# Performance work log

Measured on AMD Instinct MI355X. Metric: run time of the kernel, lower is better.

The kernel has to match this reference:

```python
import jax, jax.numpy as jnp
import numpy as np

K = 32  # attention rank
EPS = 1e-6

def setup_inputs() -> dict:
    key = jax.random.key(0)
    k1, k2 = jax.random.split(key)
    N, d = 500000, 256
    x = jax.random.normal(k1, (N, d), dtype=jnp.float32)
    # Xavier-normal-ish scale for Linear(d, 4k)
    W = jax.random.normal(k2, (d, 4 * K), dtype=jnp.float32) * jnp.sqrt(2.0 / (d + 4 * K))
    b = jnp.zeros((4 * K,), dtype=jnp.float32)
    return {"x": x, "W": W, "b": b}

def reference(x, W, b):
    # X = ReLU(x @ W + b): [N, 4k]
    X = jax.nn.relu(x @ W + b)
    U = X[:, :K]            # [N, k]
    V = X[:, K:2 * K]       # [N, k]
    Z = X[:, 2 * K:3 * K]   # [N, k]
    T = X[:, 3 * K:]        # [N, k]
    # joint_normalize2: norm_factor = sum(U @ (V^T @ ones)) / N + eps
    s = V.sum(axis=0)                              # [k] == V^T @ ones
    norm_factor = (U @ s).sum() / U.shape[0] + EPS  # scalar
    D = 1.0 / norm_factor
    # low-rank attention: U @ (V^T @ Z), inner [k, k] GEMM kept tiny
    VtZ = jnp.einsum('nk,nj->kj', V, Z)  # [k, k]
    res = U @ VtZ                        # [N, k]
    return jnp.concatenate((res * D, T), axis=1)  # [N, 2k]
```

## Files before the change

kernel.cpp:

```cpp
#include <hip/hip_runtime.h>
#include <hip/hip_bf16.h>

#define DK 256
#define NC 128
#define EPSV 1e-6f

typedef __bf16 bf16x8 __attribute__((ext_vector_type(8)));
typedef __bf16 bf16x4 __attribute__((ext_vector_type(4)));
typedef float f32x4 __attribute__((ext_vector_type(4)));


__global__ __launch_bounds__(512, 4) void k_gemm(
    const float* __restrict__ x, const float* __restrict__ W,
    const float* __restrict__ bias, float* __restrict__ out,
    float* __restrict__ accg, int N)
{
  __shared__ __bf16 Wlds[32768];
  __shared__ __bf16 Vt[32 * 72];
  __shared__ __bf16 Zt[32 * 72];
  __shared__ float  redS[64];

  const int tid  = threadIdx.x;
  const int wave = tid >> 6;
  const int lane = tid & 63;
  const int quad = lane >> 4;
  const int l16  = lane & 15;
  const int mw   = wave >> 1;
  const int nw   = wave & 1;

  for (int f = tid; f < 4096; f += 512) {
    const int n  = f & 127;
    const int qk = f >> 7;
    const int k0 = (qk >> 2) * 32 + (qk & 3) * 8;
    bf16x8 w;
    #pragma unroll
    for (int j = 0; j < 8; ++j) w[j] = (__bf16)W[(size_t)(k0 + j) * NC + n];
    *(bf16x8*)&Wlds[f * 8] = w;
  }
  float bias4[4];
  #pragma unroll
  for (int ntl = 0; ntl < 4; ++ntl) bias4[ntl] = bias[nw * 64 + ntl * 16 + l16];
  __syncthreads();

  float usumv[2] = {0.f, 0.f};
  float ssumv[2] = {0.f, 0.f};
  f32x4 vacc = (f32x4){0.f, 0.f, 0.f, 0.f};
  const int mt = wave >> 1, nt = wave & 1;

  const int nchunks = (N + 63) >> 6;
  for (int c = blockIdx.x; c < nchunks; c += gridDim.x) {
    const int rbase = c << 6;
    const int arow  = rbase + mw * 16 + l16;
    const bool rv   = arow < N;
    const float* xr = x + (size_t)arow * DK;

    f32x4 xv[16];
    #pragma unroll
    for (int kk = 0; kk < 8; ++kk) {
      const int koff = kk * 32 + quad * 8;
      xv[2 * kk]     = rv ? *(const f32x4*)(xr + koff)     : (f32x4){0.f,0.f,0.f,0.f};
      xv[2 * kk + 1] = rv ? *(const f32x4*)(xr + koff + 4) : (f32x4){0.f,0.f,0.f,0.f};
    }

    f32x4 acc[4];
    #pragma unroll
    for (int t = 0; t < 4; ++t) acc[t] = (f32x4){0.f, 0.f, 0.f, 0.f};

    #pragma unroll
    for (int kk = 0; kk < 8; ++kk) {
      bf16x8 af;
      af[0] = (__bf16)xv[2*kk].x;   af[1] = (__bf16)xv[2*kk].y;
      af[2] = (__bf16)xv[2*kk].z;   af[3] = (__bf16)xv[2*kk].w;
      af[4] = (__bf16)xv[2*kk+1].x; af[5] = (__bf16)xv[2*kk+1].y;
      af[6] = (__bf16)xv[2*kk+1].z; af[7] = (__bf16)xv[2*kk+1].w;
      #pragma unroll
      for (int ntl = 0; ntl < 4; ++ntl) {
        const bf16x8 bf = *(const bf16x8*)&Wlds[(((kk << 2) | quad) * 128
                                                + nw * 64 + ntl * 16 + l16) * 8];
        acc[ntl] = __builtin_amdgcn_mfma_f32_16x16x32_bf16(af, bf, acc[ntl], 0, 0, 0);
      }
    }

    #pragma unroll
    for (int ntl = 0; ntl < 4; ++ntl) {
      float v4[4];
      #pragma unroll
      for (int r = 0; r < 4; ++r) {
        const int grow = rbase + mw * 16 + quad * 4 + r;
        float v = acc[ntl][r] + bias4[ntl];
        v = fmaxf(v, 0.f);
        if (grow >= N) v = 0.f;
        v4[r] = v;
      }
      const int grow0 = rbase + mw * 16 + quad * 4;
      if (nw == 0) {
        if (ntl < 2) {
          #pragma unroll
          for (int r = 0; r < 4; ++r) {
            if (grow0 + r < N) out[(size_t)(grow0 + r) * 64 + ntl * 16 + l16] = v4[r];
            usumv[ntl] += v4[r];
          }
        } else {
          ssumv[ntl - 2] += v4[0] + v4[1] + v4[2] + v4[3];
          bf16x4 pv;
          pv[0] = (__bf16)v4[0]; pv[1] = (__bf16)v4[1];
          pv[2] = (__bf16)v4[2]; pv[3] = (__bf16)v4[3];
          const int col = (ntl - 2) * 16 + l16;
          const int lrow = mw * 16 + quad * 4;
          *(bf16x4*)&Vt[col * 72 + lrow] = pv;
        }
      } else {
        if (ntl < 2) {
          bf16x4 pv;
          pv[0] = (__bf16)v4[0]; pv[1] = (__bf16)v4[1];
          pv[2] = (__bf16)v4[2]; pv[3] = (__bf16)v4[3];
          const int col = ntl * 16 + l16;
          const int lrow = mw * 16 + quad * 4;
          *(bf16x4*)&Zt[col * 72 + lrow] = pv;
        } else {
          #pragma unroll
          for (int r = 0; r < 4; ++r)
            if (grow0 + r < N) out[(size_t)(grow0 + r) * 64 + 32 + (ntl - 2) * 16 + l16] = v4[r];
        }
      }
    }
    __syncthreads();
    if (wave < 4) {
      #pragma unroll
      for (int ks = 0; ks < 2; ++ks) {
        const bf16x8 av = *(const bf16x8*)&Vt[(mt * 16 + l16) * 72 + ks * 32 + quad * 8];
        const bf16x8 bz = *(const bf16x8*)&Zt[(nt * 16 + l16) * 72 + ks * 32 + quad * 8];
        vacc = __builtin_amdgcn_mfma_f32_16x16x32_bf16(av, bz, vacc, 0, 0, 0);
      }
    }
    __syncthreads();
  }

  if (tid < 64) redS[tid] = 0.f;
  __syncthreads();
  if (nw == 0) {
    atomicAdd(&redS[l16],      usumv[0]);
    atomicAdd(&redS[16 + l16], usumv[1]);
    atomicAdd(&redS[32 + l16], ssumv[0]);
    atomicAdd(&redS[48 + l16], ssumv[1]);
  }
  __syncthreads();
  if (tid < 64) atomicAdd(&accg[tid], redS[tid]);
  if (wave < 4) {
    #pragma unroll
    for (int r = 0; r < 4; ++r)
      atomicAdd(&accg[64 + (mt * 16 + quad * 4 + r) * 32 + nt * 16 + l16], vacc[r]);
  }
}

__global__ void k_norm(float* __restrict__ accg, int N) {
  const int t = threadIdx.x;
  float p = 0.f;
  if (t < 32) p = accg[t] * accg[32 + t];
  #pragma unroll
  for (int off = 16; off >= 1; off >>= 1) p += __shfl_down(p, off);
  if (t == 0) accg[1088] = 1.0f / (p / (float)N + EPSV);
}

__global__ __launch_bounds__(256) void k_res(float* __restrict__ out,
                                             const float* __restrict__ accg, int N) {
  __shared__ float Ms[32 * 33];
  __shared__ float Us[64 * 33];
  const float D = accg[1088];
  for (int i = threadIdx.x; i < 1024; i += 256)
    Ms[(i >> 5) * 33 + (i & 31)] = accg[64 + i] * D;
  const int j  = threadIdx.x & 31;
  const int r0 = threadIdx.x >> 5;
  const int rbase = blockIdx.x * 64;
  #pragma unroll
  for (int i = 0; i < 8; ++i) {
    const int lr = r0 + i * 8;
    const int row = rbase + lr;
    Us[lr * 33 + j] = (row < N) ? out[(size_t)row * 64 + j] : 0.f;
  }
  __syncthreads();
  #pragma unroll
  for (int i = 0; i < 8; ++i) {
    const int lr = r0 + i * 8;
    const int row = rbase + lr;
    if (row < N) {
      float a = 0.f;
      #pragma unroll
      for (int k = 0; k < 32; ++k) a += Us[lr * 33 + k] * Ms[k * 33 + j];
      out[(size_t)row * 64 + j] = a;
    }
  }
}

extern "C" void kernel_launch(void* const* d_in, const int* in_sizes, int n_in,
                              void* d_out, int out_size, void* d_ws, size_t ws_size,
                              hipStream_t stream) {
  const float* x    = (const float*)d_in[0];
  const float* W    = (const float*)d_in[1];
  const float* b    = (const float*)d_in[2];
  float* out  = (float*)d_out;
  float* accg = (float*)d_ws;
  const int N = in_sizes[0] / DK;
  const int ngroups = (N + 63) >> 6;

  hipMemsetAsync(accg, 0, 1089 * sizeof(float), stream);
  hipLaunchKernelGGL(k_gemm, dim3(512),     dim3(512), 0, stream, x, W, b, out, accg, N);
  hipLaunchKernelGGL(k_norm, dim3(1),       dim3(64),  0, stream, accg, N);
  hipLaunchKernelGGL(k_res,  dim3(ngroups), dim3(256), 0, stream, out, accg, N);
}
```

Measured before the change: 784.7 us.

## Give each wave full-width row tiles with private V/Z buffers, dropping per-chunk barriers

Each wave now computes all 128 output columns for its own 16 rows, using 1024-thread blocks and 256-row chunks. The V^T·Z product is accumulated from per-wave LDS scratch, so the two block-wide barriers per chunk are gone. X loads are split into two halves so the second half can overlap with the first half's MFMAs. Per-block V^T·Z partials go to workspace and a new reduction kernel sums them and computes the norm factor. In exchange it uses much more LDS and registers per block, allows only one block per CU with a 256-block grid, and adds a partial-sum write plus a reduction pass.

```diff
diff --git a/kernel.cpp b/kernel.cpp
--- a/kernel.cpp
+++ b/kernel.cpp
@@ -2,164 +2,189 @@
 #include <hip/hip_bf16.h>
 
 #define DK 256
-#define NC 128
 #define EPSV 1e-6f
+#define CHUNK 256
+#define GGRID 256
 
 typedef __bf16 bf16x8 __attribute__((ext_vector_type(8)));
 typedef __bf16 bf16x4 __attribute__((ext_vector_type(4)));
 typedef float f32x4 __attribute__((ext_vector_type(4)));
 
 
-__global__ __launch_bounds__(512, 4) void k_gemm(
+
+__global__ __launch_bounds__(1024) void k_gemm(
     const float* __restrict__ x, const float* __restrict__ W,
     const float* __restrict__ bias, float* __restrict__ out,
     float* __restrict__ accg, int N)
 {
-  __shared__ __bf16 Wlds[32768];
-  __shared__ __bf16 Vt[32 * 72];
-  __shared__ __bf16 Zt[32 * 72];
-  __shared__ float  redS[64];
+  __shared__ __align__(16) unsigned char smem[147456];
+  __bf16* Wlds = (__bf16*)smem;
 
   const int tid  = threadIdx.x;
   const int wave = tid >> 6;
   const int lane = tid & 63;
   const int quad = lane >> 4;
   const int l16  = lane & 15;
-  const int mw   = wave >> 1;
-  const int nw   = wave & 1;
-
-  for (int f = tid; f < 4096; f += 512) {
+
+  __bf16* Vsw = (__bf16*)(smem + 65536 + wave * 5120);
+  __bf16* Zsw = Vsw + 1280;
+
+  for (int i = lane; i < 2560; i += 64) Vsw[i] = (__bf16)0.f;
+
+  for (int f = tid; f < 4096; f += 1024) {
     const int n  = f & 127;
     const int qk = f >> 7;
     const int k0 = (qk >> 2) * 32 + (qk & 3) * 8;
     bf16x8 w;
     #pragma unroll
-    for (int j = 0; j < 8; ++j) w[j] = (__bf16)W[(size_t)(k0 + j) * NC + n];
+    for (int j = 0; j < 8; ++j) w[j] = (__bf16)W[(size_t)(k0 + j) * 128 + n];
     *(bf16x8*)&Wlds[f * 8] = w;
   }
-  float bias4[4];
-  #pragma unroll
-  for (int ntl = 0; ntl < 4; ++ntl) bias4[ntl] = bias[nw * 64 + ntl * 16 + l16];
-  __syncthreads();
-
-  float usumv[2] = {0.f, 0.f};
-  float ssumv[2] = {0.f, 0.f};
-  f32x4 vacc = (f32x4){0.f, 0.f, 0.f, 0.f};
-  const int mt = wave >> 1, nt = wave & 1;
-
-  const int nchunks = (N + 63) >> 6;
-  for (int c = blockIdx.x; c < nchunks; c += gridDim.x) {
-    const int rbase = c << 6;
-    const int arow  = rbase + mw * 16 + l16;
+  float bias8[8];
+  #pragma unroll
+  for (int ntl = 0; ntl < 8; ++ntl) bias8[ntl] = bias[ntl * 16 + l16];
+  __syncthreads();
+
+  float usum[2] = {0.f, 0.f};
+  float ssum[2] = {0.f, 0.f};
+  f32x4 vtz[2][2];
+  #pragma unroll
+  for (int mt = 0; mt < 2; ++mt)
+    #pragma unroll
+    for (int nt = 0; nt < 2; ++nt) vtz[mt][nt] = (f32x4){0.f, 0.f, 0.f, 0.f};
+
+  const int nch = (N + CHUNK - 1) / CHUNK;
+  for (int c = blockIdx.x; c < nch; c += gridDim.x) {
+    const int rbase = c * CHUNK + wave * 16;
+    const int arow  = rbase + l16;
     const bool rv   = arow < N;
     const float* xr = x + (size_t)arow * DK;
 
-    f32x4 xv[16];
-    #pragma unroll
-    for (int kk = 0; kk < 8; ++kk) {
-      const int koff = kk * 32 + quad * 8;
-      xv[2 * kk]     = rv ? *(const f32x4*)(xr + koff)     : (f32x4){0.f,0.f,0.f,0.f};
-      xv[2 * kk + 1] = rv ? *(const f32x4*)(xr + koff + 4) : (f32x4){0.f,0.f,0.f,0.f};
-    }
-
-    f32x4 acc[4];
-    #pragma unroll
-    for (int t = 0; t < 4; ++t) acc[t] = (f32x4){0.f, 0.f, 0.f, 0.f};
-
-    #pragma unroll
-    for (int kk = 0; kk < 8; ++kk) {
-      bf16x8 af;
-      af[0] = (__bf16)xv[2*kk].x;   af[1] = (__bf16)xv[2*kk].y;
-      af[2] = (__bf16)xv[2*kk].z;   af[3] = (__bf16)xv[2*kk].w;
-      af[4] = (__bf16)xv[2*kk+1].x; af[5] = (__bf16)xv[2*kk+1].y;
-      af[6] = (__bf16)xv[2*kk+1].z; af[7] = (__bf16)xv[2*kk+1].w;
-      #pragma unroll
-      for (int ntl = 0; ntl < 4; ++ntl) {
-        const bf16x8 bf = *(const bf16x8*)&Wlds[(((kk << 2) | quad) * 128
-                                                + nw * 64 + ntl * 16 + l16) * 8];
-        acc[ntl] = __builtin_amdgcn_mfma_f32_16x16x32_bf16(af, bf, acc[ntl], 0, 0, 0);
-      }
-    }
-
-    #pragma unroll
-    for (int ntl = 0; ntl < 4; ++ntl) {
-      float v4[4];
+    f32x4 xa[8];
+    #pragma unroll
+    for (int t = 0; t < 8; ++t)
+      xa[t] = rv ? *(const f32x4*)(xr + (t >> 1) * 32 + quad * 8 + (t & 1) * 4)
+                 : (f32x4){0.f, 0.f, 0.f, 0.f};
+
+    f32x4 acc[8];
+    #pragma unroll
+    for (int t = 0; t < 8; ++t) acc[t] = (f32x4){0.f, 0.f, 0.f, 0.f};
+
+    bf16x8 afa[4];
+    #pragma unroll
+    for (int kk = 0; kk < 4; ++kk) {
+      const f32x4 lo = xa[2 * kk], hi = xa[2 * kk + 1];
+      bf16x8 f;
+      f[0] = (__bf16)lo.x; f[1] = (__bf16)lo.y; f[2] = (__bf16)lo.z; f[3] = (__bf16)lo.w;
+      f[4] = (__bf16)hi.x; f[5] = (__bf16)hi.y; f[6] = (__bf16)hi.z; f[7] = (__bf16)hi.w;
+      afa[kk] = f;
+    }
+    f32x4 xb[8];
+    #pragma unroll
+    for (int t = 0; t < 8; ++t)
+      xb[t] = rv ? *(const f32x4*)(xr + 128 + (t >> 1) * 32 + quad * 8 + (t & 1) * 4)
+                 : (f32x4){0.f, 0.f, 0.f, 0.f};
+
+    #pragma unroll
+    for (int kk = 0; kk < 4; ++kk) {
+      #pragma unroll
+      for (int ntl = 0; ntl < 8; ++ntl) {
+        const bf16x8 bf = *(const bf16x8*)&Wlds[(((kk * 4 + quad) * 128)
+                                                + ntl * 16 + l16) * 8];
+        acc[ntl] = __builtin_amdgcn_mfma_f32_16x16x32_bf16(afa[kk], bf, acc[ntl], 0, 0, 0);
+      }
+    }
+    #pragma unroll
+    for (int kk = 4; kk < 8; ++kk) {
+      const f32x4 lo = xb[2 * (kk - 4)], hi = xb[2 * (kk - 4) + 1];
+      bf16x8 f;
+      f[0] = (__bf16)lo.x; f[1] = (__bf16)lo.y; f[2] = (__bf16)lo.z; f[3] = (__bf16)lo.w;
+      f[4] = (__bf16)hi.x; f[5] = (__bf16)hi.y; f[6] = (__bf16)hi.z; f[7] = (__bf16)hi.w;
+      #pragma unroll
+      for (int ntl = 0; ntl < 8; ++ntl) {
+        const bf16x8 bf = *(const bf16x8*)&Wlds[(((kk * 4 + quad) * 128)
+                                                + ntl * 16 + l16) * 8];
+        acc[ntl] = __builtin_amdgcn_mfma_f32_16x16x32_bf16(f, bf, acc[ntl], 0, 0, 0);
+      }
+    }
+
+    const int g0r = rbase + quad * 4;
+    #pragma unroll
+    for (int ntl = 0; ntl < 8; ++ntl) {
+      float v[4];
       #pragma unroll
       for (int r = 0; r < 4; ++r) {
-        const int grow = rbase + mw * 16 + quad * 4 + r;
-        float v = acc[ntl][r] + bias4[ntl];
-        v = fmaxf(v, 0.f);
-        if (grow >= N) v = 0.f;
-        v4[r] = v;
-      }
-      const int grow0 = rbase + mw * 16 + quad * 4;
-      if (nw == 0) {
-        if (ntl < 2) {
-          #pragma unroll
-          for (int r = 0; r < 4; ++r) {
-            if (grow0 + r < N) out[(size_t)(grow0 + r) * 64 + ntl * 16 + l16] = v4[r];
-            usumv[ntl] += v4[r];
-          }
-        } else {
-          ssumv[ntl - 2] += v4[0] + v4[1] + v4[2] + v4[3];
-          bf16x4 pv;
-          pv[0] = (__bf16)v4[0]; pv[1] = (__bf16)v4[1];
-          pv[2] = (__bf16)v4[2]; pv[3] = (__bf16)v4[3];
-          const int col = (ntl - 2) * 16 + l16;
-          const int lrow = mw * 16 + quad * 4;
-          *(bf16x4*)&Vt[col * 72 + lrow] = pv;
-        }
+        float t = fmaxf(acc[ntl][r] + bias8[ntl], 0.f);
+        v[r] = (g0r + r < N) ? t : 0.f;
+      }
+      if (ntl < 2) {
+        #pragma unroll
+        for (int r = 0; r < 4; ++r)
+          if (g0r + r < N) out[(size_t)(g0r + r) * 64 + ntl * 16 + l16] = v[r];
+        usum[ntl] += v[0] + v[1] + v[2] + v[3];
+      } else if (ntl < 4) {
+        ssum[ntl - 2] += v[0] + v[1] + v[2] + v[3];
+        bf16x4 p;
+        p[0] = (__bf16)v[0]; p[1] = (__bf16)v[1]; p[2] = (__bf16)v[2]; p[3] = (__bf16)v[3];
+        *(bf16x4*)&Vsw[((ntl - 2) * 16 + l16) * 40 + quad * 4] = p;
+      } else if (ntl < 6) {
+        bf16x4 p;
+        p[0] = (__bf16)v[0]; p[1] = (__bf16)v[1]; p[2] = (__bf16)v[2]; p[3] = (__bf16)v[3];
+        *(bf16x4*)&Zsw[((ntl - 4) * 16 + l16) * 40 + quad * 4] = p;
       } else {
-        if (ntl < 2) {
-          bf16x4 pv;
-          pv[0] = (__bf16)v4[0]; pv[1] = (__bf16)v4[1];
-          pv[2] = (__bf16)v4[2]; pv[3] = (__bf16)v4[3];
-          const int col = ntl * 16 + l16;
-          const int lrow = mw * 16 + quad * 4;
-          *(bf16x4*)&Zt[col * 72 + lrow] = pv;
-        } else {
-          #pragma unroll
-          for (int r = 0; r < 4; ++r)
-            if (grow0 + r < N) out[(size_t)(grow0 + r) * 64 + 32 + (ntl - 2) * 16 + l16] = v4[r];
-        }
-      }
-    }
-    __syncthreads();
-    if (wave < 4) {
-      #pragma unroll
-      for (int ks = 0; ks < 2; ++ks) {
-        const bf16x8 av = *(const bf16x8*)&Vt[(mt * 16 + l16) * 72 + ks * 32 + quad * 8];
-        const bf16x8 bz = *(const bf16x8*)&Zt[(nt * 16 + l16) * 72 + ks * 32 + quad * 8];
-        vacc = __builtin_amdgcn_mfma_f32_16x16x32_bf16(av, bz, vacc, 0, 0, 0);
-      }
-    }
-    __syncthreads();
-  }
-
+        #pragma unroll
+        for (int r = 0; r < 4; ++r)
+          if (g0r + r < N) out[(size_t)(g0r + r) * 64 + 32 + (ntl - 6) * 16 + l16] = v[r];
+      }
+    }
+
+    #pragma unroll
+    for (int mt = 0; mt < 2; ++mt) {
+      const bf16x8 av = *(const bf16x8*)&Vsw[(mt * 16 + l16) * 40 + quad * 8];
+      #pragma unroll
+      for (int nt = 0; nt < 2; ++nt) {
+        const bf16x8 bz = *(const bf16x8*)&Zsw[(nt * 16 + l16) * 40 + quad * 8];
+        vtz[mt][nt] = __builtin_amdgcn_mfma_f32_16x16x32_bf16(av, bz, vtz[mt][nt], 0, 0, 0);
+      }
+    }
+  }
+
+  __syncthreads();
+  float* vtzL = (float*)(smem + 65536);
+  float* redS = vtzL + 1024;
+  vtzL[tid] = 0.f;
   if (tid < 64) redS[tid] = 0.f;
   __syncthreads();
-  if (nw == 0) {
-    atomicAdd(&redS[l16],      usumv[0]);
-    atomicAdd(&redS[16 + l16], usumv[1]);
-    atomicAdd(&redS[32 + l16], ssumv[0]);
-    atomicAdd(&redS[48 + l16], ssumv[1]);
-  }
+  atomicAdd(&redS[l16],      usum[0]);
+  atomicAdd(&redS[16 + l16], usum[1]);
+  atomicAdd(&redS[32 + l16], ssum[0]);
+  atomicAdd(&redS[48 + l16], ssum[1]);
+  #pragma unroll
+  for (int mt = 0; mt < 2; ++mt)
+    #pragma unroll
+    for (int nt = 0; nt < 2; ++nt)
+      #pragma unroll
+      for (int r = 0; r < 4; ++r)
+        atomicAdd(&vtzL[(mt * 16 + quad * 4 + r) * 32 + nt * 16 + l16], vtz[mt][nt][r]);
   __syncthreads();
   if (tid < 64) atomicAdd(&accg[tid], redS[tid]);
-  if (wave < 4) {
-    #pragma unroll
-    for (int r = 0; r < 4; ++r)
-      atomicAdd(&accg[64 + (mt * 16 + quad * 4 + r) * 32 + nt * 16 + l16], vacc[r]);
-  }
-}
-
-__global__ void k_norm(float* __restrict__ accg, int N) {
-  const int t = threadIdx.x;
-  float p = 0.f;
-  if (t < 32) p = accg[t] * accg[32 + t];
-  #pragma unroll
-  for (int off = 16; off >= 1; off >>= 1) p += __shfl_down(p, off);
-  if (t == 0) accg[1088] = 1.0f / (p / (float)N + EPSV);
+  accg[4096 + blockIdx.x * 1024 + tid] = vtzL[tid];
+}
+
+__global__ __launch_bounds__(256) void k_red(float* __restrict__ accg, int N, int nblocks) {
+  const int gid = blockIdx.x * 256 + threadIdx.x;
+  const float* part = accg + 4096;
+  float a = 0.f;
+  #pragma unroll 8
+  for (int b = 0; b < nblocks; ++b) a += part[b * 1024 + gid];
+  accg[64 + gid] = a;
+  if (blockIdx.x == 0 && threadIdx.x < 64) {
+    const int l = threadIdx.x;
+    float p = (l < 32) ? accg[l] * accg[32 + l] : 0.f;
+    #pragma unroll
+    for (int off = 32; off >= 1; off >>= 1) p += __shfl_down(p, off);
+    if (l == 0) accg[1088] = 1.0f / (p / (float)N + EPSV);
+  }
 }
 
 __global__ __launch_bounds__(256) void k_res(float* __restrict__ out,
@@ -204,7 +229,7 @@
   const int ngroups = (N + 63) >> 6;
 
   hipMemsetAsync(accg, 0, 1089 * sizeof(float), stream);
-  hipLaunchKernelGGL(k_gemm, dim3(512),     dim3(512), 0, stream, x, W, b, out, accg, N);
-  hipLaunchKernelGGL(k_norm, dim3(1),       dim3(64),  0, stream, accg, N);
-  hipLaunchKernelGGL(k_res,  dim3(ngroups), dim3(256), 0, stream, out, accg, N);
-}
+  hipLaunchKernelGGL(k_gemm, dim3(GGRID),   dim3(1024), 0, stream, x, W, b, out, accg, N);
+  hipLaunchKernelGGL(k_red,  dim3(4),       dim3(256),  0, stream, accg, N, GGRID);
+  hipLaunchKernelGGL(k_res,  dim3(ngroups), dim3(256),  0, stream, out, accg, N);
+}
```

After: 808.2 us. 3.0% more time.
